# Kernel optimization log

Hardware: AMD Instinct MI355X
Metric: run time of the kernel (lower is better)

Reference implementation:

```python
import jax, jax.numpy as jnp
import numpy as np

B, N_IN, NODE, L = 4, 128, 32, 256
N_HID, N_OUT = 64, 128
D_IN = N_HID          # d_inner = expand(1) * d_model
D_STATE = 2 * N_HID   # d_state = n_hid * 2
D_CONV = 2
DT_RANK = max(1, -(-N_HID // 16))  # ceil(d_model/16) = 4


def setup_inputs() -> dict:
    key = jax.random.key(0)
    ks = jax.random.split(key, 12)
    s = lambda k, shape, scale: (jax.random.normal(k, shape, jnp.float32) * scale)
    inputs = jax.random.normal(ks[0], (B, N_IN, NODE, L), jnp.float32)
    return {
        "inputs": inputs,
        "w_in": s(ks[1], (N_HID, N_IN), 1.0 / np.sqrt(N_IN)),
        "b_in": jnp.zeros((N_HID,), jnp.float32),
        "in_proj_w": s(ks[2], (2 * D_IN, N_HID), 1.0 / np.sqrt(N_HID)),
        "conv_w": s(ks[3], (D_IN, D_CONV), 0.5),
        "conv_b": jnp.zeros((D_IN,), jnp.float32),
        "x_proj_w": s(ks[4], (DT_RANK + 2 * D_STATE, D_IN), 1.0 / np.sqrt(D_IN)),
        "dt_proj_w": s(ks[5], (D_IN, DT_RANK), DT_RANK ** -0.5),
        "dt_proj_b": s(ks[6], (D_IN,), 0.1),
        "A_log": jnp.log(jnp.tile(jnp.arange(1, D_STATE + 1, dtype=jnp.float32)[None, :], (D_IN, 1))),
        "D": jnp.ones((D_IN,), jnp.float32),
        "out_proj_w": s(ks[7], (N_HID, D_IN), 1.0 / np.sqrt(D_IN)),
        "w_out": s(ks[8], (N_OUT, N_HID), 1.0 / np.sqrt(N_HID)),
        "b_out": jnp.zeros((N_OUT,), jnp.float32),
        "ln_w": jnp.ones((L, N_OUT), jnp.float32),
        "ln_b": jnp.zeros((L, N_OUT), jnp.float32),
    }


def _mamba(x, in_proj_w, conv_w, conv_b, x_proj_w, dt_proj_w, dt_proj_b, A_log, D, out_proj_w):
    # x: (Bseq, L, d_model)
    Bs, Ls, _ = x.shape
    d_state = A_log.shape[1]
    dt_rank = dt_proj_w.shape[1]
    d_conv = conv_w.shape[1]

    xz = x @ in_proj_w.T                     # (Bs, L, 2*d_inner)
    xm, z = jnp.split(xz, 2, axis=-1)

    # causal depthwise conv1d (padding = d_conv-1, truncated to L)
    xp = jnp.pad(xm, ((0, 0), (d_conv - 1, 0), (0, 0)))
    xc = sum(xp[:, k:k + Ls, :] * conv_w[:, k] for k in range(d_conv)) + conv_b
    xc = jax.nn.silu(xc)                     # (Bs, L, d_inner)

    dbc = xc @ x_proj_w.T                    # (Bs, L, dt_rank + 2*d_state)
    dt = dbc[..., :dt_rank]
    Bm = dbc[..., dt_rank:dt_rank + d_state]
    Cm = dbc[..., dt_rank + d_state:]
    delta = jax.nn.softplus(dt @ dt_proj_w.T + dt_proj_b)  # (Bs, L, d_inner)
    A = -jnp.exp(A_log)                      # (d_inner, d_state)

    def step(h, inp):
        dlt, Bt, Ct, xt = inp                # (Bs,d), (Bs,s), (Bs,s), (Bs,d)
        dA = jnp.exp(dlt[:, :, None] * A)    # (Bs, d, s)
        h = dA * h + (dlt * xt)[:, :, None] * Bt[:, None, :]
        y = jnp.einsum('bds,bs->bd', h, Ct)
        return h, y

    h0 = jnp.zeros((Bs, xm.shape[-1], d_state), x.dtype)
    xs = (delta.transpose(1, 0, 2), Bm.transpose(1, 0, 2),
          Cm.transpose(1, 0, 2), xc.transpose(1, 0, 2))
    _, ys = jax.lax.scan(step, h0, xs)       # ys: (L, Bs, d_inner)

    y = ys.transpose(1, 0, 2) + xc * D
    y = y * jax.nn.silu(z)
    return y @ out_proj_w.T                  # (Bs, L, d_model)


def reference(inputs, w_in, b_in, in_proj_w, conv_w, conv_b, x_proj_w,
              dt_proj_w, dt_proj_b, A_log, D, out_proj_w,
              w_out, b_out, ln_w, ln_b):
    b, n_in, node, seq = inputs.shape
    # permute(0,2,3,1).reshape(B*node, L, n_in)
    x = inputs.transpose(0, 2, 3, 1).reshape(b * node, seq, n_in)
    x = x @ w_in.T + b_in
    x = jax.nn.silu(_mamba(x, in_proj_w, conv_w, conv_b, x_proj_w,
                           dt_proj_w, dt_proj_b, A_log, D, out_proj_w))
    x = x @ w_out.T + b_out                  # (B*node, L, n_out)
    # LayerNorm over last two dims [feature_len, n_out]
    mu = x.mean(axis=(-2, -1), keepdims=True)
    var = ((x - mu) ** 2).mean(axis=(-2, -1), keepdims=True)
    x = (x - mu) / jnp.sqrt(var + 1e-5) * ln_w + ln_b
    return x.reshape(b, node, seq, -1).transpose(0, 3, 1, 2)
```

## Files before the change

kernel.cpp:

```cpp
#include <hip/hip_runtime.h>
#include <math.h>


__device__ __forceinline__ float silu_f(float v) { return v / (1.f + __expf(-v)); }
__device__ __forceinline__ float softplus_f(float v) { return v > 20.f ? v : log1pf(__expf(v)); }

#if __has_builtin(__builtin_amdgcn_exp2f)
#define EXP2N(x) __builtin_amdgcn_exp2f(x)
#else
#define EXP2N(x) __expf((x) * 0.6931471805599453f)
#endif

__global__ __launch_bounds__(256) void k1_proj(
    const float* __restrict__ inp, const float* __restrict__ w_in,
    const float* __restrict__ b_in, const float* __restrict__ ipw,
    float* __restrict__ XM, float* __restrict__ Zb)
{
  __shared__ float sIN[128*64];
  __shared__ float sW[64*68];
  __shared__ float sXT[64*68];
  const int bid = blockIdx.x;
  const int r = bid >> 2, tb = bid & 3;
  const int b = r >> 5, node = r & 31;
  const int t0 = tb * 64;
  const int tid = threadIdx.x;
  const int tg = tid & 15, vg = tid >> 4;
  const int tl0 = tg * 4, v0 = vg * 4;

  for (int e = tid; e < 128*64; e += 256) {
    int i = e >> 6, t = e & 63;
    sIN[e] = inp[((b*128 + i)*32 + node)*256 + t0 + t];
  }

  float acc[4][4];
  #pragma unroll
  for (int ti = 0; ti < 4; ti++)
    #pragma unroll
    for (int j = 0; j < 4; j++) acc[ti][j] = b_in[v0 + j];

  for (int kc = 0; kc < 2; kc++) {
    __syncthreads();
    for (int e = tid; e < 64*16; e += 256) {
      int row = e >> 4, c4 = e & 15;
      *(float4*)&sW[row*68 + c4*4] = *(const float4*)&w_in[row*128 + kc*64 + c4*4];
    }
    __syncthreads();
    for (int k4 = 0; k4 < 16; k4++) {
      float4 wv[4];
      #pragma unroll
      for (int j = 0; j < 4; j++)
        wv[j] = *(const float4*)&sW[(v0 + j)*68 + k4*4];
      #pragma unroll
      for (int kk = 0; kk < 4; kk++) {
        float4 x4 = *(const float4*)&sIN[(kc*64 + k4*4 + kk)*64 + tl0];
        #pragma unroll
        for (int j = 0; j < 4; j++) {
          float w = kk==0 ? wv[j].x : kk==1 ? wv[j].y : kk==2 ? wv[j].z : wv[j].w;
          acc[0][j] = fmaf(x4.x, w, acc[0][j]);
          acc[1][j] = fmaf(x4.y, w, acc[1][j]);
          acc[2][j] = fmaf(x4.z, w, acc[2][j]);
          acc[3][j] = fmaf(x4.w, w, acc[3][j]);
        }
      }
    }
  }
  #pragma unroll
  for (int j = 0; j < 4; j++)
    *(float4*)&sXT[(v0 + j)*68 + tl0] =
        make_float4(acc[0][j], acc[1][j], acc[2][j], acc[3][j]);

  for (int pass = 0; pass < 2; pass++) {
    __syncthreads();
    for (int e = tid; e < 64*16; e += 256) {
      int row = e >> 4, c4 = e & 15;
      *(float4*)&sW[row*68 + c4*4] = *(const float4*)&ipw[(pass*64 + row)*64 + c4*4];
    }
    __syncthreads();

    float a2[4][4];
    #pragma unroll
    for (int ti = 0; ti < 4; ti++)
      #pragma unroll
      for (int j = 0; j < 4; j++) a2[ti][j] = 0.f;

    for (int k4 = 0; k4 < 16; k4++) {
      float4 wv[4];
      #pragma unroll
      for (int j = 0; j < 4; j++)
        wv[j] = *(const float4*)&sW[(v0 + j)*68 + k4*4];
      #pragma unroll
      for (int kk = 0; kk < 4; kk++) {
        float4 x4 = *(const float4*)&sXT[(k4*4 + kk)*68 + tl0];
        #pragma unroll
        for (int j = 0; j < 4; j++) {
          float w = kk==0 ? wv[j].x : kk==1 ? wv[j].y : kk==2 ? wv[j].z : wv[j].w;
          a2[0][j] = fmaf(x4.x, w, a2[0][j]);
          a2[1][j] = fmaf(x4.y, w, a2[1][j]);
          a2[2][j] = fmaf(x4.z, w, a2[2][j]);
          a2[3][j] = fmaf(x4.w, w, a2[3][j]);
        }
      }
    }

    if (pass == 0) {
      #pragma unroll
      for (int ti = 0; ti < 4; ti++)
        *(float4*)&XM[(r*256 + t0 + tl0 + ti)*64 + v0] =
            make_float4(a2[ti][0], a2[ti][1], a2[ti][2], a2[ti][3]);
    } else {
      #pragma unroll
      for (int j = 0; j < 4; j++)
        *(float4*)&Zb[(r*64 + v0 + j)*256 + t0 + tl0] =
            make_float4(a2[0][j], a2[1][j], a2[2][j], a2[3][j]);
    }
  }
}

__global__ __launch_bounds__(256) void k2_conv_xproj(
    const float* __restrict__ XM, const float* __restrict__ convw,
    const float* __restrict__ convb, const float* __restrict__ xpw,
    const float* __restrict__ dtw, const float* __restrict__ dtb,
    float* __restrict__ XC, float* __restrict__ DELTA,
    float* __restrict__ BM, float* __restrict__ CM)
{
  __shared__ float sXM[65*64];
  __shared__ float sXC[64*68];
  __shared__ float sW[64*68];
  __shared__ float sDT[64*5];
  const int bid = blockIdx.x;
  const int r = bid >> 2, tb = bid & 3;
  const int t0 = tb * 64;
  const int tid = threadIdx.x;
  const int tg = tid & 15, vg = tid >> 4;
  const int tl0 = tg * 4, v0 = vg * 4;

  for (int e = tid; e < 65*64; e += 256) {
    int tt = e >> 6, d = e & 63;
    int tgl = t0 - 1 + tt;
    sXM[e] = (tgl < 0) ? 0.f : XM[(r*256 + tgl)*64 + d];
  }
  __syncthreads();

  for (int e = tid; e < 64*64; e += 256) {
    int t = e >> 6, d = e & 63;
    float c0 = convw[d*2], c1 = convw[d*2 + 1];
    float pre = fmaf(sXM[t*64 + d], c0, fmaf(sXM[(t+1)*64 + d], c1, convb[d]));
    sXC[d*68 + t] = silu_f(pre);
  }
  __syncthreads();

  for (int e = tid; e < 64*64; e += 256) {
    int d = e >> 6, t = e & 63;
    XC[(r*64 + d)*256 + t0 + t] = sXC[d*68 + t];
  }

  for (int pass = 0; pass < 5; pass++) {
    __syncthreads();
    for (int e = tid; e < 64*16; e += 256) {
      int row = e >> 4, c4 = e & 15;
      int grow = pass*64 + row;
      float4 w = (grow < 260) ? *(const float4*)&xpw[grow*64 + c4*4]
                              : make_float4(0.f, 0.f, 0.f, 0.f);
      *(float4*)&sW[row*68 + c4*4] = w;
    }
    __syncthreads();

    float acc[4][4];
    #pragma unroll
    for (int ti = 0; ti < 4; ti++)
      #pragma unroll
      for (int jj = 0; jj < 4; jj++) acc[ti][jj] = 0.f;

    for (int k4 = 0; k4 < 16; k4++) {
      float4 wv[4];
      #pragma unroll
      for (int jj = 0; jj < 4; jj++)
        wv[jj] = *(const float4*)&sW[(v0 + jj)*68 + k4*4];
      #pragma unroll
      for (int kk = 0; kk < 4; kk++) {
        float4 x4 = *(const float4*)&sXC[(k4*4 + kk)*68 + tl0];
        #pragma unroll
        for (int jj = 0; jj < 4; jj++) {
          float w = kk==0 ? wv[jj].x : kk==1 ? wv[jj].y : kk==2 ? wv[jj].z : wv[jj].w;
          acc[0][jj] = fmaf(x4.x, w, acc[0][jj]);
          acc[1][jj] = fmaf(x4.y, w, acc[1][jj]);
          acc[2][jj] = fmaf(x4.z, w, acc[2][jj]);
          acc[3][jj] = fmaf(x4.w, w, acc[3][jj]);
        }
      }
    }

    const int j0g = pass*64 + v0;
    if (j0g < 4) {
      #pragma unroll
      for (int ti = 0; ti < 4; ti++)
        #pragma unroll
        for (int jj = 0; jj < 4; jj++)
          sDT[(tl0 + ti)*5 + jj] = acc[ti][jj];
    } else if (j0g < 132) {
      #pragma unroll
      for (int ti = 0; ti < 4; ti++)
        *(float4*)&BM[(r*256 + t0 + tl0 + ti)*128 + (j0g - 4)] =
            make_float4(acc[ti][0], acc[ti][1], acc[ti][2], acc[ti][3]);
    } else if (j0g < 260) {
      #pragma unroll
      for (int ti = 0; ti < 4; ti++)
        *(float4*)&CM[(r*256 + t0 + tl0 + ti)*128 + (j0g - 132)] =
            make_float4(acc[ti][0], acc[ti][1], acc[ti][2], acc[ti][3]);
    }
  }
  __syncthreads();

  for (int e = tid; e < 64*64; e += 256) {
    int d = e >> 6, t = e & 63;
    float4 w4 = *(const float4*)&dtw[d*4];
    float x = dtb[d];
    x = fmaf(sDT[t*5 + 0], w4.x, x);
    x = fmaf(sDT[t*5 + 1], w4.y, x);
    x = fmaf(sDT[t*5 + 2], w4.z, x);
    x = fmaf(sDT[t*5 + 3], w4.w, x);
    DELTA[(r*64 + d)*256 + t0 + t] = softplus_f(x);
  }
}

__global__ __launch_bounds__(256) void k3_scan(
    const float* __restrict__ DELTA, const float* __restrict__ XC,
    const float* __restrict__ BM, const float* __restrict__ CM,
    const float* __restrict__ alog, float* __restrict__ YP)
{
  const int bid = blockIdx.x;
  const int r = bid & 127;
  const int rest = bid >> 7;
  const int sc = rest & 1;
  const int dc = rest >> 1;
  const int tid = threadIdx.x;
  const int dg = tid >> 4;
  const int sg = tid & 15;
  const int sl0 = sg * 4;
  const int d = dc*16 + dg;
  const float LOG2E = 1.44269504f;

  float a2[4], h[4];
  #pragma unroll
  for (int j = 0; j < 4; j++) {
    a2[j] = -expf(alog[d*128 + sc*64 + sl0 + j]) * LOG2E;
    h[j] = 0.f;
  }

  const float* pB = BM    + r*256*128 + sc*64 + sl0;
  const float* pC = CM    + r*256*128 + sc*64 + sl0;
  const float* pD = DELTA + ((size_t)(r*64 + d))*256;
  const float* pX = XC    + ((size_t)(r*64 + d))*256;
  float*       pY = YP + ((size_t)((sc*128 + r)*64 + d))*256;

  float4 vB0, vC0, vB1, vC1, vB2, vC2, vB3, vC3;

#define K3_LDBC(SET, T_) do { \
    vB##SET = *(const float4*)(pB + (T_)*128); \
    vC##SET = *(const float4*)(pC + (T_)*128); \
  } while (0)

#define K3_STEP(SET, DL_, XV_, YOUT_) do { \
    float dl = (DL_), xv = (XV_); \
    float4 Bv = vB##SET, Cv = vC##SET; \
    float u = dl * xv; \
    float y; \
    float dA0 = EXP2N(dl * a2[0]); \
    h[0] = fmaf(dA0, h[0], u * Bv.x); \
    y = h[0] * Cv.x; \
    float dA1 = EXP2N(dl * a2[1]); \
    h[1] = fmaf(dA1, h[1], u * Bv.y); \
    y = fmaf(h[1], Cv.y, y); \
    float dA2 = EXP2N(dl * a2[2]); \
    h[2] = fmaf(dA2, h[2], u * Bv.z); \
    y = fmaf(h[2], Cv.z, y); \
    float dA3 = EXP2N(dl * a2[3]); \
    h[3] = fmaf(dA3, h[3], u * Bv.w); \
    y = fmaf(h[3], Cv.w, y); \
    int yi; \
    yi = __builtin_amdgcn_update_dpp(__float_as_int(y), __float_as_int(y), \
                                     0x121, 0xf, 0xf, false); \
    y += __int_as_float(yi); \
    yi = __builtin_amdgcn_update_dpp(__float_as_int(y), __float_as_int(y), \
                                     0x122, 0xf, 0xf, false); \
    y += __int_as_float(yi); \
    yi = __builtin_amdgcn_update_dpp(__float_as_int(y), __float_as_int(y), \
                                     0x124, 0xf, 0xf, false); \
    y += __int_as_float(yi); \
    yi = __builtin_amdgcn_update_dpp(__float_as_int(y), __float_as_int(y), \
                                     0x128, 0xf, 0xf, false); \
    y += __int_as_float(yi); \
    (YOUT_) = y; \
  } while (0)

  float4 d4c = *(const float4*)(pD + 0);
  float4 x4c = *(const float4*)(pX + 0);
  K3_LDBC(0, 0); K3_LDBC(1, 1); K3_LDBC(2, 2); K3_LDBC(3, 3);

  for (int t = 0; t < 256; t += 4) {
    float4 d4n, x4n;
    if (t < 252) {
      d4n = *(const float4*)(pD + t + 4);
      x4n = *(const float4*)(pX + t + 4);
    }
    float4 yv;
    K3_STEP(0, d4c.x, x4c.x, yv.x); if (t < 252) K3_LDBC(0, t + 4);
    K3_STEP(1, d4c.y, x4c.y, yv.y); if (t < 252) K3_LDBC(1, t + 5);
    K3_STEP(2, d4c.z, x4c.z, yv.z); if (t < 252) K3_LDBC(2, t + 6);
    K3_STEP(3, d4c.w, x4c.w, yv.w); if (t < 252) K3_LDBC(3, t + 7);
    if (sg == 0)
      *(float4*)(pY + t) = yv;
    if (t < 252) { d4c = d4n; x4c = x4n; }
  }

#undef K3_LDBC
#undef K3_STEP
}

__global__ __launch_bounds__(256) void k4_post(
    const float* __restrict__ YP, const float* __restrict__ XC,
    const float* __restrict__ Zb, const float* __restrict__ Dp,
    const float* __restrict__ opw, const float* __restrict__ wout,
    const float* __restrict__ bout, float* __restrict__ out,
    float* __restrict__ PSTAT)
{
  __shared__ float sY[64*68];
  __shared__ float sU[64*68];
  __shared__ float sW[64*68];
  __shared__ float sRs[256], sRq[256];
  const int bid = blockIdx.x;
  const int r = bid >> 2, tb = bid & 3;
  const int b = r >> 5, node = r & 31;
  const int t0 = tb * 64;
  const int tid = threadIdx.x;
  const int tg = tid & 15, vg = tid >> 4;
  const int tl0 = tg * 4, v0 = vg * 4;

  for (int e = tid; e < 64*64; e += 256) {
    int d = e >> 6, t = e & 63;
    int idxT = (r*64 + d)*256 + t0 + t;
    float y = YP[idxT] + YP[2097152 + idxT];
    float y2 = fmaf(XC[idxT], Dp[d], y);
    sY[d*68 + t] = y2 * silu_f(Zb[idxT]);
  }

  __syncthreads();
  for (int e = tid; e < 64*16; e += 256) {
    int row = e >> 4, c4 = e & 15;
    *(float4*)&sW[row*68 + c4*4] = *(const float4*)&opw[row*64 + c4*4];
  }
  __syncthreads();

  {
    float acc[4][4];
    #pragma unroll
    for (int ti = 0; ti < 4; ti++)
      #pragma unroll
      for (int j = 0; j < 4; j++) acc[ti][j] = 0.f;
    for (int k4 = 0; k4 < 16; k4++) {
      float4 wv[4];
      #pragma unroll
      for (int j = 0; j < 4; j++)
        wv[j] = *(const float4*)&sW[(v0 + j)*68 + k4*4];
      #pragma unroll
      for (int kk = 0; kk < 4; kk++) {
        float4 x4 = *(const float4*)&sY[(k4*4 + kk)*68 + tl0];
        #pragma unroll
        for (int j = 0; j < 4; j++) {
          float w = kk==0 ? wv[j].x : kk==1 ? wv[j].y : kk==2 ? wv[j].z : wv[j].w;
          acc[0][j] = fmaf(x4.x, w, acc[0][j]);
          acc[1][j] = fmaf(x4.y, w, acc[1][j]);
          acc[2][j] = fmaf(x4.z, w, acc[2][j]);
          acc[3][j] = fmaf(x4.w, w, acc[3][j]);
        }
      }
    }
    #pragma unroll
    for (int j = 0; j < 4; j++)
      *(float4*)&sU[(v0 + j)*68 + tl0] =
          make_float4(silu_f(acc[0][j]), silu_f(acc[1][j]),
                      silu_f(acc[2][j]), silu_f(acc[3][j]));
  }

  float s = 0.f, q = 0.f;
  for (int pass = 0; pass < 2; pass++) {
    __syncthreads();
    for (int e = tid; e < 64*16; e += 256) {
      int row = e >> 4, c4 = e & 15;
      *(float4*)&sW[row*68 + c4*4] = *(const float4*)&wout[(pass*64 + row)*64 + c4*4];
    }
    __syncthreads();

    float a2[4][4];
    #pragma unroll
    for (int ti = 0; ti < 4; ti++)
      #pragma unroll
      for (int j = 0; j < 4; j++) a2[ti][j] = bout[pass*64 + v0 + j];

    for (int k4 = 0; k4 < 16; k4++) {
      float4 wv[4];
      #pragma unroll
      for (int j = 0; j < 4; j++)
        wv[j] = *(const float4*)&sW[(v0 + j)*68 + k4*4];
      #pragma unroll
      for (int kk = 0; kk < 4; kk++) {
        float4 x4 = *(const float4*)&sU[(k4*4 + kk)*68 + tl0];
        #pragma unroll
        for (int j = 0; j < 4; j++) {
          float w = kk==0 ? wv[j].x : kk==1 ? wv[j].y : kk==2 ? wv[j].z : wv[j].w;
          a2[0][j] = fmaf(x4.x, w, a2[0][j]);
          a2[1][j] = fmaf(x4.y, w, a2[1][j]);
          a2[2][j] = fmaf(x4.z, w, a2[2][j]);
          a2[3][j] = fmaf(x4.w, w, a2[3][j]);
        }
      }
    }

    #pragma unroll
    for (int ti = 0; ti < 4; ti++)
      #pragma unroll
      for (int j = 0; j < 4; j++) {
        float v = a2[ti][j];
        s += v;
        q = fmaf(v, v, q);
      }
    #pragma unroll
    for (int j = 0; j < 4; j++) {
      int o = pass*64 + v0 + j;
      *(float4*)&out[((b*128 + o)*32 + node)*256 + t0 + tl0] =
          make_float4(a2[0][j], a2[1][j], a2[2][j], a2[3][j]);
    }
  }

  sRs[tid] = s; sRq[tid] = q;
  __syncthreads();
  for (int st = 128; st > 0; st >>= 1) {
    if (tid < st) { sRs[tid] += sRs[tid + st]; sRq[tid] += sRq[tid + st]; }
    __syncthreads();
  }
  if (tid == 0) { PSTAT[bid*2] = sRs[0]; PSTAT[bid*2 + 1] = sRq[0]; }
}

__global__ __launch_bounds__(256) void k5_ln(
    const float* __restrict__ PSTAT, const float* __restrict__ lnw,
    const float* __restrict__ lnb, float* __restrict__ out)
{
  __shared__ float sLW[32*129], sLB[32*129];
  const int bid = blockIdx.x;
  const int r = bid >> 3, tb = bid & 7;
  const int b = r >> 5, node = r & 31;
  const int t0 = tb * 32;
  const int tid = threadIdx.x;

  float s = 0.f, q = 0.f;
  #pragma unroll
  for (int p = 0; p < 4; p++) {
    s += PSTAT[(r*4 + p)*2];
    q += PSTAT[(r*4 + p)*2 + 1];
  }
  const float mu = s * (1.f / 32768.f);
  const float var = q * (1.f / 32768.f) - mu * mu;
  const float rstd = rsqrtf(var + 1e-5f);

  for (int e = tid; e < 32*128; e += 256) {
    int t = e >> 7, o = e & 127;
    sLW[t*129 + o] = lnw[(t0 + t)*128 + o];
    sLB[t*129 + o] = lnb[(t0 + t)*128 + o];
  }
  __syncthreads();

  for (int n = 0; n < 16; n++) {
    int t = tid & 31;
    int o = (tid >> 5) + n*8;
    int idx = ((b*128 + o)*32 + node)*256 + t0 + t;
    float v = out[idx];
    out[idx] = fmaf((v - mu) * rstd, sLW[t*129 + o], sLB[t*129 + o]);
  }
}

extern "C" void kernel_launch(void* const* d_in, const int* in_sizes, int n_in,
                              void* d_out, int out_size, void* d_ws, size_t ws_size,
                              hipStream_t stream)
{
  (void)in_sizes; (void)n_in; (void)out_size; (void)ws_size;
  const float* inp   = (const float*)d_in[0];
  const float* w_in  = (const float*)d_in[1];
  const float* b_in  = (const float*)d_in[2];
  const float* ipw   = (const float*)d_in[3];
  const float* convw = (const float*)d_in[4];
  const float* convb = (const float*)d_in[5];
  const float* xpw   = (const float*)d_in[6];
  const float* dtw   = (const float*)d_in[7];
  const float* dtb   = (const float*)d_in[8];
  const float* alog  = (const float*)d_in[9];
  const float* Dp    = (const float*)d_in[10];
  const float* opw   = (const float*)d_in[11];
  const float* wout  = (const float*)d_in[12];
  const float* bout  = (const float*)d_in[13];
  const float* lnw   = (const float*)d_in[14];
  const float* lnb   = (const float*)d_in[15];

  float* ws = (float*)d_ws;
  float* XM    = ws + 0;
  float* Zb    = ws + 2097152;
  float* XC    = ws + 4194304;
  float* DELTA = ws + 6291456;
  float* BM    = ws + 8388608;
  float* CM    = ws + 12582912;
  float* YP    = ws + 16777216;
  float* PSTAT = ws + 20971520;
  float* out   = (float*)d_out;

  k1_proj<<<dim3(512), dim3(256), 0, stream>>>(inp, w_in, b_in, ipw, XM, Zb);
  k2_conv_xproj<<<dim3(512), dim3(256), 0, stream>>>(XM, convw, convb, xpw, dtw, dtb,
                                                     XC, DELTA, BM, CM);
  k3_scan<<<dim3(1024), dim3(256), 0, stream>>>(DELTA, XC, BM, CM, alog, YP);
  k4_post<<<dim3(512), dim3(256), 0, stream>>>(YP, XC, Zb, Dp, opw, wout, bout, out, PSTAT);
  k5_ln<<<dim3(1024), dim3(256), 0, stream>>>(PSTAT, lnw, lnb, out);
}
```

Before: 183.3 us.

## Split scan state across 32 lanes per channel with two states each

```diff
diff --git a/kernel.cpp b/kernel.cpp
--- a/kernel.cpp
+++ b/kernel.cpp
@@ -223,7 +223,7 @@
   }
 }
 
-__global__ __launch_bounds__(256) void k3_scan(
+__global__ __launch_bounds__(512, 8) void k3_scan(
     const float* __restrict__ DELTA, const float* __restrict__ XC,
     const float* __restrict__ BM, const float* __restrict__ CM,
     const float* __restrict__ alog, float* __restrict__ YP)
@@ -234,18 +234,16 @@
   const int sc = rest & 1;
   const int dc = rest >> 1;
   const int tid = threadIdx.x;
-  const int dg = tid >> 4;
-  const int sg = tid & 15;
-  const int sl0 = sg * 4;
+  const int dg = tid >> 5;
+  const int sg = tid & 31;
+  const int sl0 = sg * 2;
   const int d = dc*16 + dg;
   const float LOG2E = 1.44269504f;
 
-  float a2[4], h[4];
-  #pragma unroll
-  for (int j = 0; j < 4; j++) {
-    a2[j] = -expf(alog[d*128 + sc*64 + sl0 + j]) * LOG2E;
-    h[j] = 0.f;
-  }
+  float a20, a21, h0, h1;
+  a20 = -expf(alog[d*128 + sc*64 + sl0 + 0]) * LOG2E;
+  a21 = -expf(alog[d*128 + sc*64 + sl0 + 1]) * LOG2E;
+  h0 = 0.f; h1 = 0.f;
 
   const float* pB = BM    + r*256*128 + sc*64 + sl0;
   const float* pC = CM    + r*256*128 + sc*64 + sl0;
@@ -253,42 +251,40 @@
   const float* pX = XC    + ((size_t)(r*64 + d))*256;
   float*       pY = YP + ((size_t)((sc*128 + r)*64 + d))*256;
 
-  float4 vB0, vC0, vB1, vC1, vB2, vC2, vB3, vC3;
+  float2 vB0, vC0, vB1, vC1, vB2, vC2, vB3, vC3;
 
 #define K3_LDBC(SET, T_) do { \
-    vB##SET = *(const float4*)(pB + (T_)*128); \
-    vC##SET = *(const float4*)(pC + (T_)*128); \
+    vB##SET = *(const float2*)(pB + (T_)*128); \
+    vC##SET = *(const float2*)(pC + (T_)*128); \
   } while (0)
 
 #define K3_STEP(SET, DL_, XV_, YOUT_) do { \
     float dl = (DL_), xv = (XV_); \
-    float4 Bv = vB##SET, Cv = vC##SET; \
+    float2 Bv = vB##SET, Cv = vC##SET; \
     float u = dl * xv; \
     float y; \
-    float dA0 = EXP2N(dl * a2[0]); \
-    h[0] = fmaf(dA0, h[0], u * Bv.x); \
-    y = h[0] * Cv.x; \
-    float dA1 = EXP2N(dl * a2[1]); \
-    h[1] = fmaf(dA1, h[1], u * Bv.y); \
-    y = fmaf(h[1], Cv.y, y); \
-    float dA2 = EXP2N(dl * a2[2]); \
-    h[2] = fmaf(dA2, h[2], u * Bv.z); \
-    y = fmaf(h[2], Cv.z, y); \
-    float dA3 = EXP2N(dl * a2[3]); \
-    h[3] = fmaf(dA3, h[3], u * Bv.w); \
-    y = fmaf(h[3], Cv.w, y); \
+    float dA0 = EXP2N(dl * a20); \
+    h0 = fmaf(dA0, h0, u * Bv.x); \
+    y = h0 * Cv.x; \
+    float dA1 = EXP2N(dl * a21); \
+    h1 = fmaf(dA1, h1, u * Bv.y); \
+    y = fmaf(h1, Cv.y, y); \
     int yi; \
     yi = __builtin_amdgcn_update_dpp(__float_as_int(y), __float_as_int(y), \
-                                     0x121, 0xf, 0xf, false); \
+                                     0x121, 0xf, 0xf, false);   \
     y += __int_as_float(yi); \
     yi = __builtin_amdgcn_update_dpp(__float_as_int(y), __float_as_int(y), \
-                                     0x122, 0xf, 0xf, false); \
+                                     0x122, 0xf, 0xf, false);   \
     y += __int_as_float(yi); \
     yi = __builtin_amdgcn_update_dpp(__float_as_int(y), __float_as_int(y), \
-                                     0x124, 0xf, 0xf, false); \
+                                     0x124, 0xf, 0xf, false);   \
     y += __int_as_float(yi); \
     yi = __builtin_amdgcn_update_dpp(__float_as_int(y), __float_as_int(y), \
-                                     0x128, 0xf, 0xf, false); \
+                                     0x128, 0xf, 0xf, false);   \
+    y += __int_as_float(yi); \
+     \
+    yi = __builtin_amdgcn_update_dpp(__float_as_int(y), __float_as_int(y), \
+                                     0x142, 0xf, 0xf, false);   \
     y += __int_as_float(yi); \
     (YOUT_) = y; \
   } while (0)
@@ -308,7 +304,7 @@
     K3_STEP(1, d4c.y, x4c.y, yv.y); if (t < 252) K3_LDBC(1, t + 5);
     K3_STEP(2, d4c.z, x4c.z, yv.z); if (t < 252) K3_LDBC(2, t + 6);
     K3_STEP(3, d4c.w, x4c.w, yv.w); if (t < 252) K3_LDBC(3, t + 7);
-    if (sg == 0)
+    if (sg == 16)
       *(float4*)(pY + t) = yv;
     if (t < 252) { d4c = d4n; x4c = x4n; }
   }
@@ -514,7 +510,7 @@
   k1_proj<<<dim3(512), dim3(256), 0, stream>>>(inp, w_in, b_in, ipw, XM, Zb);
   k2_conv_xproj<<<dim3(512), dim3(256), 0, stream>>>(XM, convw, convb, xpw, dtw, dtb,
                                                      XC, DELTA, BM, CM);
-  k3_scan<<<dim3(1024), dim3(256), 0, stream>>>(DELTA, XC, BM, CM, alog, YP);
+  k3_scan<<<dim3(1024), dim3(512), 0, stream>>>(DELTA, XC, BM, CM, alog, YP);
   k4_post<<<dim3(512), dim3(256), 0, stream>>>(YP, XC, Zb, Dp, opw, wout, bout, out, PSTAT);
   k5_ln<<<dim3(1024), dim3(256), 0, stream>>>(PSTAT, lnw, lnb, out);
 }
```

Measured after the change: 259.2 us. 1.41x slower.
